# Kernel optimization log

Hardware: AMD Instinct MI355X
Metric: run time of the kernel (lower is better)

Reference implementation:

```python
import jax, jax.numpy as jnp
import numpy as np

# bitsandbytes NF4 codebook (16 levels)
NF4_CODE = jnp.array([
    -1.0, -0.6961928009986877, -0.5250730514526367, -0.39491748809814453,
    -0.28444138169288635, -0.18477343022823334, -0.09105003625154495, 0.0,
    0.07958029955625534, 0.16093020141124725, 0.24611230194568634,
    0.33791524171829224, 0.44070982933044434, 0.5626170039176941,
    0.7229568362236023, 1.0], dtype=jnp.float32)

IN_F, OUT_F, BLOCK = 4096, 16384, 64

def setup_inputs() -> dict:
    key = jax.random.key(0)
    k1, k2, k3 = jax.random.split(key, 3)
    x = jax.random.normal(k1, (8, 1, IN_F), dtype=jnp.float32)
    codes = jax.random.randint(k2, (OUT_F, IN_F), 0, 16, dtype=jnp.int32)
    absmax = jax.random.uniform(k3, (OUT_F, IN_F // BLOCK), dtype=jnp.float32)
    return {"x": x, "codes": codes, "absmax": absmax}

def reference(x, codes, absmax):
    out_f, in_f = codes.shape
    n_blocks = absmax.shape[1]
    bs = in_f // n_blocks
    # blockwise dequantize: w[o, b*bs + j] = codebook[code] * absmax[o, b]
    w = NF4_CODE[codes].reshape(out_f, n_blocks, bs) * absmax[:, :, None]
    w = w.reshape(out_f, in_f)  # [out, in], the full dequantized weight
    # F.linear(x, w) = x @ w.T
    return jnp.einsum('bti,oi->bto', x, w)
```

## Files before the change

kernel.cpp:

```cpp
#include <hip/hip_runtime.h>


#define IN_F   4096
#define OUT_F  16384
#define NBLK   64
#define ROWS   8
#define BATCH  8
#define K_VEC  (IN_F / 4)
#define K_ITER (K_VEC / 64)

__device__ __constant__ float NF4_CODE_C[16] = {
    -1.0f, -0.6961928009986877f, -0.5250730514526367f, -0.39491748809814453f,
    -0.28444138169288635f, -0.18477343022823334f, -0.09105003625154495f, 0.0f,
    0.07958029955625534f, 0.16093020141124725f, 0.24611230194568634f,
    0.33791524171829224f, 0.44070982933044434f, 0.5626170039176941f,
    0.7229568362236023f, 1.0f};

__global__ __launch_bounds__(256, 2) void nf4_gemv(
    const float* __restrict__ x,
    const int* __restrict__ codes,
    const float* __restrict__ absmax,
    float* __restrict__ out)
{
    __shared__ float lut[16];
    if (threadIdx.x < 16) lut[threadIdx.x] = NF4_CODE_C[threadIdx.x];
    __syncthreads();

    const int lane   = threadIdx.x & 63;
    const int wave   = threadIdx.x >> 6;
    const int gwave  = blockIdx.x * 4 + wave;
    const int o_base = gwave * ROWS;

    const int4*   codes4 = (const int4*)codes;
    const float4* x4     = (const float4*)x;

    float a_reg[ROWS];
#pragma unroll
    for (int r = 0; r < ROWS; ++r)
        a_reg[r] = absmax[(size_t)(o_base + r) * NBLK + lane];

    float acc[ROWS][BATCH];
#pragma unroll
    for (int r = 0; r < ROWS; ++r)
#pragma unroll
        for (int b = 0; b < BATCH; ++b) acc[r][b] = 0.0f;

    for (int t = 0; t < K_ITER; ++t) {
        const int vec = t * 64 + lane;

        int4 cr[ROWS];
#pragma unroll
        for (int r = 0; r < ROWS; ++r)
            cr[r] = codes4[(size_t)(o_base + r) * K_VEC + vec];

        float4 xv[BATCH];
#pragma unroll
        for (int b = 0; b < BATCH; ++b)
            xv[b] = x4[b * K_VEC + vec];

#pragma unroll
        for (int r = 0; r < ROWS; ++r) {
            const float am = __shfl(a_reg[r], t * 4 + (lane >> 4), 64);
            const float w0 = lut[cr[r].x & 15] * am;
            const float w1 = lut[cr[r].y & 15] * am;
            const float w2 = lut[cr[r].z & 15] * am;
            const float w3 = lut[cr[r].w & 15] * am;
#pragma unroll
            for (int b = 0; b < BATCH; ++b) {
                float s = acc[r][b];
                s = fmaf(w0, xv[b].x, s);
                s = fmaf(w1, xv[b].y, s);
                s = fmaf(w2, xv[b].z, s);
                s = fmaf(w3, xv[b].w, s);
                acc[r][b] = s;
            }
        }
    }

#pragma unroll
    for (int r = 0; r < ROWS; ++r)
#pragma unroll
        for (int b = 0; b < BATCH; ++b) {
            float v = acc[r][b];
#pragma unroll
            for (int off = 32; off > 0; off >>= 1)
                v += __shfl_xor(v, off, 64);
            acc[r][b] = v;
        }

    if (lane == 0) {
#pragma unroll
        for (int r = 0; r < ROWS; ++r)
#pragma unroll
            for (int b = 0; b < BATCH; ++b)
                out[b * OUT_F + o_base + r] = acc[r][b];
    }
}

extern "C" void kernel_launch(void* const* d_in, const int* in_sizes, int n_in,
                              void* d_out, int out_size, void* d_ws, size_t ws_size,
                              hipStream_t stream) {
    const float* x      = (const float*)d_in[0];
    const int*   codes  = (const int*)d_in[1];
    const float* absmax = (const float*)d_in[2];
    float*       out    = (float*)d_out;

    dim3 grid(OUT_F / (ROWS * 4));
    dim3 block(256);
    nf4_gemv<<<grid, block, 0, stream>>>(x, codes, absmax, out);
}
```

Baseline: 367.0 us.

## Halve rows per wave, double-buffer code loads, bank-spread LUT, LDS-based reduction

```diff
diff --git a/kernel.cpp b/kernel.cpp
--- a/kernel.cpp
+++ b/kernel.cpp
@@ -4,8 +4,9 @@
 #define IN_F   4096
 #define OUT_F  16384
 #define NBLK   64
-#define ROWS   8
+#define ROWS   4
 #define BATCH  8
+#define WAVES  4
 #define K_VEC  (IN_F / 4)
 #define K_ITER (K_VEC / 64)
 
@@ -16,20 +17,22 @@
     0.33791524171829224f, 0.44070982933044434f, 0.5626170039176941f,
     0.7229568362236023f, 1.0f};
 
-__global__ __launch_bounds__(256, 2) void nf4_gemv(
+__global__ __launch_bounds__(256, 3) void nf4_gemv(
     const float* __restrict__ x,
     const int* __restrict__ codes,
     const float* __restrict__ absmax,
     float* __restrict__ out)
 {
-    __shared__ float lut[16];
-    if (threadIdx.x < 16) lut[threadIdx.x] = NF4_CODE_C[threadIdx.x];
+    __shared__ float lut2[16 * 64];
+    __shared__ float red[WAVES][32 * 64];
+
+    for (int j = threadIdx.x; j < 16 * 64; j += 256)
+        lut2[j] = NF4_CODE_C[j >> 6];
     __syncthreads();
 
     const int lane   = threadIdx.x & 63;
     const int wave   = threadIdx.x >> 6;
-    const int gwave  = blockIdx.x * 4 + wave;
-    const int o_base = gwave * ROWS;
+    const int o_base = (blockIdx.x * WAVES + wave) * ROWS;
 
     const int4*   codes4 = (const int4*)codes;
     const float4* x4     = (const float4*)x;
@@ -45,56 +48,102 @@
 #pragma unroll
         for (int b = 0; b < BATCH; ++b) acc[r][b] = 0.0f;
 
-    for (int t = 0; t < K_ITER; ++t) {
-        const int vec = t * 64 + lane;
+    const int4* crow[ROWS];
+#pragma unroll
+    for (int r = 0; r < ROWS; ++r)
+        crow[r] = codes4 + (size_t)(o_base + r) * K_VEC + lane;
 
-        int4 cr[ROWS];
+    const float* lutl = lut2 + lane;
+
+    int4 crA[ROWS], crB[ROWS];
+#pragma unroll
+    for (int r = 0; r < ROWS; ++r) crA[r] = crow[r][0];
+
+    float4 xv[BATCH];
+
+#pragma unroll 1
+    for (int i = 0; i < K_ITER / 2; ++i) {
+        const int tA = 2 * i;
+        const int tB = 2 * i + 1;
+
+#pragma unroll
+        for (int b = 0; b < BATCH; ++b)
+            xv[b] = x4[b * K_VEC + tA * 64 + lane];
 #pragma unroll
         for (int r = 0; r < ROWS; ++r)
-            cr[r] = codes4[(size_t)(o_base + r) * K_VEC + vec];
+            crB[r] = crow[r][tB * 64];
 
-        float4 xv[BATCH];
+        {
+            const int bi = tA * 4 + (lane >> 4);
+#pragma unroll
+            for (int r = 0; r < ROWS; ++r) {
+                const float am = __shfl(a_reg[r], bi, 64);
+                const float w0 = lutl[(crA[r].x & 15) << 6] * am;
+                const float w1 = lutl[(crA[r].y & 15) << 6] * am;
+                const float w2 = lutl[(crA[r].z & 15) << 6] * am;
+                const float w3 = lutl[(crA[r].w & 15) << 6] * am;
+#pragma unroll
+                for (int b = 0; b < BATCH; ++b) {
+                    float s = acc[r][b];
+                    s = fmaf(w0, xv[b].x, s);
+                    s = fmaf(w1, xv[b].y, s);
+                    s = fmaf(w2, xv[b].z, s);
+                    s = fmaf(w3, xv[b].w, s);
+                    acc[r][b] = s;
+                }
+            }
+        }
+
 #pragma unroll
         for (int b = 0; b < BATCH; ++b)
-            xv[b] = x4[b * K_VEC + vec];
+            xv[b] = x4[b * K_VEC + tB * 64 + lane];
+        if (i < K_ITER / 2 - 1) {
+#pragma unroll
+            for (int r = 0; r < ROWS; ++r)
+                crA[r] = crow[r][(tB + 1) * 64];
+        }
 
+        {
+            const int bi = tB * 4 + (lane >> 4);
 #pragma unroll
-        for (int r = 0; r < ROWS; ++r) {
-            const float am = __shfl(a_reg[r], t * 4 + (lane >> 4), 64);
-            const float w0 = lut[cr[r].x & 15] * am;
-            const float w1 = lut[cr[r].y & 15] * am;
-            const float w2 = lut[cr[r].z & 15] * am;
-            const float w3 = lut[cr[r].w & 15] * am;
+            for (int r = 0; r < ROWS; ++r) {
+                const float am = __shfl(a_reg[r], bi, 64);
+                const float w0 = lutl[(crB[r].x & 15) << 6] * am;
+                const float w1 = lutl[(crB[r].y & 15) << 6] * am;
+                const float w2 = lutl[(crB[r].z & 15) << 6] * am;
+                const float w3 = lutl[(crB[r].w & 15) << 6] * am;
 #pragma unroll
-            for (int b = 0; b < BATCH; ++b) {
-                float s = acc[r][b];
-                s = fmaf(w0, xv[b].x, s);
-                s = fmaf(w1, xv[b].y, s);
-                s = fmaf(w2, xv[b].z, s);
-                s = fmaf(w3, xv[b].w, s);
-                acc[r][b] = s;
+                for (int b = 0; b < BATCH; ++b) {
+                    float s = acc[r][b];
+                    s = fmaf(w0, xv[b].x, s);
+                    s = fmaf(w1, xv[b].y, s);
+                    s = fmaf(w2, xv[b].z, s);
+                    s = fmaf(w3, xv[b].w, s);
+                    acc[r][b] = s;
+                }
             }
         }
     }
 
+    float* myred = &red[wave][0];
 #pragma unroll
     for (int r = 0; r < ROWS; ++r)
 #pragma unroll
-        for (int b = 0; b < BATCH; ++b) {
-            float v = acc[r][b];
+        for (int b = 0; b < BATCH; ++b)
+            myred[(b * ROWS + r) * 64 + lane] = acc[r][b];
+
+    __asm__ volatile("s_waitcnt lgkmcnt(0)" ::: "memory");
+
+    const int p = lane & 31;
+    const int h = lane >> 5;
+    float v = 0.0f;
 #pragma unroll
-            for (int off = 32; off > 0; off >>= 1)
-                v += __shfl_xor(v, off, 64);
-            acc[r][b] = v;
-        }
+    for (int j = 0; j < 32; ++j)
+        v += myred[p * 64 + h * 32 + ((j + p) & 31)];
+    v += __shfl_xor(v, 32, 64);
 
-    if (lane == 0) {
-#pragma unroll
-        for (int r = 0; r < ROWS; ++r)
-#pragma unroll
-            for (int b = 0; b < BATCH; ++b)
-                out[b * OUT_F + o_base + r] = acc[r][b];
-    }
+    if (lane < 32)
+        out[(size_t)(p >> 2) * OUT_F + o_base + (p & 3)] = v;
 }
 
 extern "C" void kernel_launch(void* const* d_in, const int* in_sizes, int n_in,
@@ -105,7 +154,7 @@
     const float* absmax = (const float*)d_in[2];
     float*       out    = (float*)d_out;
 
-    dim3 grid(OUT_F / (ROWS * 4));
+    dim3 grid(OUT_F / (ROWS * WAVES));
     dim3 block(256);
     nf4_gemv<<<grid, block, 0, stream>>>(x, codes, absmax, out);
 }
```

After: 369.8 us. No clear change (+0.8%).
